# Optimization experiments

Measured on AMD Instinct MI355X. Metric: run time of the kernel, lower is better.

The kernel has to match this reference:

```python
import jax, jax.numpy as jnp
import numpy as np

B, S, I, H = 64, 1024, 512, 512


def setup_inputs() -> dict:
    key = jax.random.key(0)
    ks = jax.random.split(key, 6)
    stdv = 1.0 / np.sqrt(H)
    return {
        "inputs": jax.random.normal(ks[0], (B, S, I), dtype=jnp.float32),
        "h0": jax.random.normal(ks[1], (1, B, H), dtype=jnp.float32),
        "weight_ih": jax.random.uniform(ks[2], (H, I), jnp.float32, -stdv, stdv),
        "weight_hh": jax.random.uniform(ks[3], (H, H), jnp.float32, -stdv, stdv),
        "bias_ih": jax.random.uniform(ks[4], (H,), jnp.float32, -stdv, stdv),
        "bias_hh": jax.random.uniform(ks[5], (H,), jnp.float32, -stdv, stdv),
    }


def reference(inputs, h0, weight_ih, weight_hh, bias_ih, bias_hh):
    batch = inputs.shape[0]
    hidd = bias_hh.shape[0]
    # Precompute the input projection for all timesteps in one big GEMM:
    # [B, S, I] @ [I, H] -> [B, S, H], plus both biases.
    x_proj = jnp.einsum("bsi,hi->bsh", inputs, weight_ih) + bias_ih + bias_hh
    h_init = h0.reshape(batch, hidd)

    def step(h_prev, xp_t):  # xp_t: [B, H]
        h_t = jax.nn.relu(xp_t + h_prev @ weight_hh.T)
        return h_t, h_t

    h_final, outs = jax.lax.scan(step, h_init, jnp.swapaxes(x_proj, 0, 1))
    outputs = jnp.swapaxes(outs, 0, 1)  # [B, S, H]
    return outputs, h_final[None, :, :]
```

## Files before the change

kernel.cpp:

```cpp
#include <hip/hip_runtime.h>

#define B_ 64
#define S_ 1024
#define I_ 512
#define H_ 512
#define SH_ (S_ * H_)
#define OUT_H (B_ * SH_)

__global__ __launch_bounds__(256) void xproj_kernel(
    const float* __restrict__ A, const float* __restrict__ W,
    const float* __restrict__ bih, const float* __restrict__ bhh,
    float* __restrict__ out)
{
  __shared__ float As[16][132];
  __shared__ float Bs[16][132];
  const int tid = threadIdx.x;
  const int m0 = blockIdx.x * 128;
  const int n0 = blockIdx.y * 128;

  float acc[8][8];
  #pragma unroll
  for (int i = 0; i < 8; ++i)
    #pragma unroll
    for (int j = 0; j < 8; ++j) acc[i][j] = 0.f;

  const int mb = (tid >> 4) * 8;
  const int nb = (tid & 15) * 8;

  for (int kb = 0; kb < I_ / 16; ++kb) {
    const int k0 = kb * 16;
    __syncthreads();
    #pragma unroll
    for (int l = 0; l < 2; ++l) {
      int s  = tid + l * 256;
      int ml = s >> 2;
      int kc = s & 3;
      float4 av = *(const float4*)(A + (size_t)(m0 + ml) * I_ + k0 + kc * 4);
      As[kc*4+0][ml] = av.x; As[kc*4+1][ml] = av.y;
      As[kc*4+2][ml] = av.z; As[kc*4+3][ml] = av.w;
      float4 bv = *(const float4*)(W + (size_t)(n0 + ml) * I_ + k0 + kc * 4);
      Bs[kc*4+0][ml] = bv.x; Bs[kc*4+1][ml] = bv.y;
      Bs[kc*4+2][ml] = bv.z; Bs[kc*4+3][ml] = bv.w;
    }
    __syncthreads();
    #pragma unroll
    for (int k = 0; k < 16; ++k) {
      float4 a0 = *(const float4*)&As[k][mb];
      float4 a1 = *(const float4*)&As[k][mb + 4];
      float4 b0 = *(const float4*)&Bs[k][nb];
      float4 b1 = *(const float4*)&Bs[k][nb + 4];
      float a[8] = {a0.x,a0.y,a0.z,a0.w,a1.x,a1.y,a1.z,a1.w};
      float b[8] = {b0.x,b0.y,b0.z,b0.w,b1.x,b1.y,b1.z,b1.w};
      #pragma unroll
      for (int i = 0; i < 8; ++i)
        #pragma unroll
        for (int j = 0; j < 8; ++j) acc[i][j] += a[i] * b[j];
    }
  }

  float bias[8];
  #pragma unroll
  for (int j = 0; j < 8; ++j) bias[j] = bih[n0 + nb + j] + bhh[n0 + nb + j];
  #pragma unroll
  for (int i = 0; i < 8; ++i) {
    float4 v0 = make_float4(acc[i][0]+bias[0], acc[i][1]+bias[1],
                            acc[i][2]+bias[2], acc[i][3]+bias[3]);
    float4 v1 = make_float4(acc[i][4]+bias[4], acc[i][5]+bias[5],
                            acc[i][6]+bias[6], acc[i][7]+bias[7]);
    float* o = out + (size_t)(m0 + mb + i) * H_ + n0 + nb;
    *(float4*)o       = v0;
    *(float4*)(o + 4) = v1;
  }
}

__global__ __launch_bounds__(256) void init_kernel(unsigned* __restrict__ hbu)
{
  int i = blockIdx.x * 256 + threadIdx.x;
  if (i < B_ * H_) hbu[i] = 0u;
}

__global__ __launch_bounds__(512, 1) void recur_kernel(
    const float* __restrict__ Whh, const float* __restrict__ h0,
    float* __restrict__ out, unsigned* __restrict__ hbu)
{
  const int tid   = threadIdx.x;
  const int bg    = blockIdx.x & 31;
  const int ns    = blockIdx.x >> 5;
  const int b0    = bg * 2;
  const int obase = ns * 64;
  const int o4    = tid & 15;
  const int kq    = tid >> 4;

  __shared__ float hsh[2 * H_];
  __shared__ float red[32][132];

  float Wr[4][16];
  #pragma unroll
  for (int i = 0; i < 4; ++i) {
    const float4* wrow =
        (const float4*)(Whh + (size_t)(obase + o4 * 4 + i) * H_ + kq * 16);
    #pragma unroll
    for (int j = 0; j < 4; ++j) {
      float4 w4 = wrow[j];
      Wr[i][4*j+0] = w4.x; Wr[i][4*j+1] = w4.y;
      Wr[i][4*j+2] = w4.z; Wr[i][4*j+3] = w4.w;
    }
  }

  const int ep   = tid >> 6;
  const int lane = tid & 63;
  float* outp = out + (size_t)(b0 + ep) * SH_ + obase + lane;

  for (int t = 0; t < S_; ++t) {
    float xp = 0.f;
    if (tid < 128) xp = *outp;

    if (t == 0) {
      const float* hp = h0 + b0 * H_;
      hsh[tid]       = hp[tid];
      hsh[tid + 512] = hp[tid + 512];
    } else {
      const unsigned* hs = hbu + (t & 1) * (B_ * H_) + b0 * H_;
      const unsigned expct = ((unsigned)t >> 1) & 1u;
      unsigned a0 = __hip_atomic_load(hs + tid,       __ATOMIC_RELAXED,
                                      __HIP_MEMORY_SCOPE_AGENT);
      unsigned a1 = __hip_atomic_load(hs + tid + 512, __ATOMIC_RELAXED,
                                      __HIP_MEMORY_SCOPE_AGENT);
      while ((a0 >> 31) != expct) {
        __builtin_amdgcn_s_sleep(1);
        a0 = __hip_atomic_load(hs + tid, __ATOMIC_RELAXED,
                               __HIP_MEMORY_SCOPE_AGENT);
      }
      while ((a1 >> 31) != expct) {
        __builtin_amdgcn_s_sleep(1);
        a1 = __hip_atomic_load(hs + tid + 512, __ATOMIC_RELAXED,
                               __HIP_MEMORY_SCOPE_AGENT);
      }
      hsh[tid]       = __uint_as_float(a0 & 0x7fffffffu);
      hsh[tid + 512] = __uint_as_float(a1 & 0x7fffffffu);
    }
    __syncthreads();

    float acc[2][4] = {{0.f,0.f,0.f,0.f},{0.f,0.f,0.f,0.f}};
    #pragma unroll
    for (int b = 0; b < 2; ++b) {
      const float* hp = hsh + b * H_ + kq * 16;
      #pragma unroll
      for (int j = 0; j < 16; ++j) {
        float hv = hp[j];
        #pragma unroll
        for (int i = 0; i < 4; ++i) acc[b][i] += hv * Wr[i][j];
      }
    }

    #pragma unroll
    for (int b = 0; b < 2; ++b)
      *(float4*)&red[kq][b * 64 + o4 * 4] =
          make_float4(acc[b][0], acc[b][1], acc[b][2], acc[b][3]);
    __syncthreads();

    if (tid < 128) {
      float s = 0.f;
      #pragma unroll
      for (int q = 0; q < 32; ++q) s += red[q][ep * 64 + lane];
      float v = xp + s;
      v = v > 0.f ? v : 0.f;
      const unsigned tg = ((((unsigned)(t + 1)) >> 1) & 1u) << 31;
      unsigned* hd = hbu + ((t + 1) & 1) * (B_ * H_) + (b0 + ep) * H_
                   + obase + lane;
      __hip_atomic_store(hd, __float_as_uint(v) | tg,
                         __ATOMIC_RELAXED, __HIP_MEMORY_SCOPE_AGENT);
      *outp = v;
      if (t == S_ - 1)
        out[(size_t)OUT_H + (b0 + ep) * H_ + obase + lane] = v;
      outp += H_;
    }
  }
}

extern "C" void kernel_launch(void* const* d_in, const int* in_sizes, int n_in,
                              void* d_out, int out_size, void* d_ws, size_t ws_size,
                              hipStream_t stream)
{
  const float* inputs = (const float*)d_in[0];
  const float* h0     = (const float*)d_in[1];
  const float* w_ih   = (const float*)d_in[2];
  const float* w_hh   = (const float*)d_in[3];
  const float* b_ih   = (const float*)d_in[4];
  const float* b_hh   = (const float*)d_in[5];
  float* out = (float*)d_out;

  unsigned* hbu = (unsigned*)d_ws;

  dim3 g1(512, 4);
  xproj_kernel<<<g1, 256, 0, stream>>>(inputs, w_ih, b_ih, b_hh, out);
  init_kernel<<<128, 256, 0, stream>>>(hbu);
  recur_kernel<<<256, 512, 0, stream>>>(w_hh, h0, out, hbu);
}
```

Baseline: 2.236 ms.

## Restructure recurrence so each wavefront owns one batch row and reduces via shuffles

The recurrent kernel is remapped so each block handles a single batch row and each wavefront independently computes 16 output features over the full hidden dimension. Every wave polls and loads the whole previous hidden vector into its own shared-memory slice, and the K-split partial sums are combined with cross-lane shuffles. This removes both block-wide __syncthreads and the shared-memory reduction from every timestep. In exchange each wave issues eight times more polling loads, the register-held weight slice doubles in size, and launch bounds now target two blocks per CU.

Result: slower. 6.587 ms (+194.6%).

```diff
diff --git a/kernel.cpp b/kernel.cpp
--- a/kernel.cpp
+++ b/kernel.cpp
@@ -79,100 +79,114 @@
   if (i < B_ * H_) hbu[i] = 0u;
 }
 
-__global__ __launch_bounds__(512, 1) void recur_kernel(
+__global__ __launch_bounds__(512, 2) void recur_kernel(
     const float* __restrict__ Whh, const float* __restrict__ h0,
     float* __restrict__ out, unsigned* __restrict__ hbu)
 {
   const int tid   = threadIdx.x;
-  const int bg    = blockIdx.x & 31;
-  const int ns    = blockIdx.x >> 5;
-  const int b0    = bg * 2;
-  const int obase = ns * 64;
-  const int o4    = tid & 15;
-  const int kq    = tid >> 4;
-
-  __shared__ float hsh[2 * H_];
-  __shared__ float red[32][132];
-
-  float Wr[4][16];
+  const int lane  = tid & 63;
+  const int w     = tid >> 6;
+  const int b     = blockIdx.x & 63;
+  const int sub   = blockIdx.x >> 6;
+  const int wv    = sub * 8 + w;
+  const int obase = wv * 16;
+  const int og    = lane & 3;
+  const int kg    = lane >> 2;
+
+  __shared__ float hsh[8][16 * 36];
+
+  float Wr[4][32];
   #pragma unroll
   for (int i = 0; i < 4; ++i) {
     const float4* wrow =
-        (const float4*)(Whh + (size_t)(obase + o4 * 4 + i) * H_ + kq * 16);
-    #pragma unroll
-    for (int j = 0; j < 4; ++j) {
+        (const float4*)(Whh + (size_t)(obase + og * 4 + i) * H_ + kg * 32);
+    #pragma unroll
+    for (int j = 0; j < 8; ++j) {
       float4 w4 = wrow[j];
       Wr[i][4*j+0] = w4.x; Wr[i][4*j+1] = w4.y;
       Wr[i][4*j+2] = w4.z; Wr[i][4*j+3] = w4.w;
     }
   }
 
-  const int ep   = tid >> 6;
-  const int lane = tid & 63;
-  float* outp = out + (size_t)(b0 + ep) * SH_ + obase + lane;
+  float* hls  = &hsh[w][0];
+  float* outp = out + (size_t)b * SH_ + obase + og * 4;
 
   for (int t = 0; t < S_; ++t) {
-    float xp = 0.f;
-    if (tid < 128) xp = *outp;
+    float4 xp = make_float4(0.f, 0.f, 0.f, 0.f);
+    if (lane < 4) xp = *(const float4*)outp;
 
     if (t == 0) {
-      const float* hp = h0 + b0 * H_;
-      hsh[tid]       = hp[tid];
-      hsh[tid + 512] = hp[tid + 512];
+      const float* hp = h0 + b * H_;
+      #pragma unroll
+      for (int j = 0; j < 8; ++j) {
+        int e = lane + 64 * j;
+        hls[(e >> 5) * 36 + (e & 31)] = hp[e];
+      }
     } else {
-      const unsigned* hs = hbu + (t & 1) * (B_ * H_) + b0 * H_;
+      const unsigned* hs = hbu + (t & 1) * (B_ * H_) + b * H_;
       const unsigned expct = ((unsigned)t >> 1) & 1u;
-      unsigned a0 = __hip_atomic_load(hs + tid,       __ATOMIC_RELAXED,
-                                      __HIP_MEMORY_SCOPE_AGENT);
-      unsigned a1 = __hip_atomic_load(hs + tid + 512, __ATOMIC_RELAXED,
-                                      __HIP_MEMORY_SCOPE_AGENT);
-      while ((a0 >> 31) != expct) {
-        __builtin_amdgcn_s_sleep(1);
-        a0 = __hip_atomic_load(hs + tid, __ATOMIC_RELAXED,
-                               __HIP_MEMORY_SCOPE_AGENT);
+      unsigned a[8];
+      #pragma unroll
+      for (int j = 0; j < 8; ++j)
+        a[j] = __hip_atomic_load(hs + lane + 64 * j, __ATOMIC_RELAXED,
+                                 __HIP_MEMORY_SCOPE_AGENT);
+      #pragma unroll
+      for (int j = 0; j < 8; ++j) {
+        while ((a[j] >> 31) != expct) {
+          __builtin_amdgcn_s_sleep(1);
+          a[j] = __hip_atomic_load(hs + lane + 64 * j, __ATOMIC_RELAXED,
+                                   __HIP_MEMORY_SCOPE_AGENT);
+        }
+        int e = lane + 64 * j;
+        hls[(e >> 5) * 36 + (e & 31)] = __uint_as_float(a[j] & 0x7fffffffu);
       }
-      while ((a1 >> 31) != expct) {
-        __builtin_amdgcn_s_sleep(1);
-        a1 = __hip_atomic_load(hs + tid + 512, __ATOMIC_RELAXED,
-                               __HIP_MEMORY_SCOPE_AGENT);
+    }
+    asm volatile("s_waitcnt lgkmcnt(0)" ::: "memory");
+
+    float ac[4] = {0.f, 0.f, 0.f, 0.f};
+    const float* hc = hls + kg * 36;
+    #pragma unroll
+    for (int j4 = 0; j4 < 8; ++j4) {
+      float4 hv = *(const float4*)(hc + 4 * j4);
+      #pragma unroll
+      for (int i = 0; i < 4; ++i) {
+        ac[i] += hv.x * Wr[i][4*j4+0];
+        ac[i] += hv.y * Wr[i][4*j4+1];
+        ac[i] += hv.z * Wr[i][4*j4+2];
+        ac[i] += hv.w * Wr[i][4*j4+3];
       }
-      hsh[tid]       = __uint_as_float(a0 & 0x7fffffffu);
-      hsh[tid + 512] = __uint_as_float(a1 & 0x7fffffffu);
-    }
-    __syncthreads();
-
-    float acc[2][4] = {{0.f,0.f,0.f,0.f},{0.f,0.f,0.f,0.f}};
-    #pragma unroll
-    for (int b = 0; b < 2; ++b) {
-      const float* hp = hsh + b * H_ + kq * 16;
-      #pragma unroll
-      for (int j = 0; j < 16; ++j) {
-        float hv = hp[j];
-        #pragma unroll
-        for (int i = 0; i < 4; ++i) acc[b][i] += hv * Wr[i][j];
-      }
-    }
-
-    #pragma unroll
-    for (int b = 0; b < 2; ++b)
-      *(float4*)&red[kq][b * 64 + o4 * 4] =
-          make_float4(acc[b][0], acc[b][1], acc[b][2], acc[b][3]);
-    __syncthreads();
-
-    if (tid < 128) {
-      float s = 0.f;
-      #pragma unroll
-      for (int q = 0; q < 32; ++q) s += red[q][ep * 64 + lane];
-      float v = xp + s;
-      v = v > 0.f ? v : 0.f;
+    }
+
+    #pragma unroll
+    for (int i = 0; i < 4; ++i) {
+      float r = ac[i];
+      r += __shfl_xor(r, 4);
+      r += __shfl_xor(r, 8);
+      r += __shfl_xor(r, 16);
+      r += __shfl_xor(r, 32);
+      ac[i] = r;
+    }
+
+    if (lane < 4) {
+      float4 v;
+      v.x = fmaxf(xp.x + ac[0], 0.f);
+      v.y = fmaxf(xp.y + ac[1], 0.f);
+      v.z = fmaxf(xp.z + ac[2], 0.f);
+      v.w = fmaxf(xp.w + ac[3], 0.f);
       const unsigned tg = ((((unsigned)(t + 1)) >> 1) & 1u) << 31;
-      unsigned* hd = hbu + ((t + 1) & 1) * (B_ * H_) + (b0 + ep) * H_
-                   + obase + lane;
-      __hip_atomic_store(hd, __float_as_uint(v) | tg,
-                         __ATOMIC_RELAXED, __HIP_MEMORY_SCOPE_AGENT);
-      *outp = v;
+      unsigned* hd = hbu + ((t + 1) & 1) * (B_ * H_) + b * H_
+                   + obase + og * 4;
+      __hip_atomic_store(hd + 0, __float_as_uint(v.x) | tg,
+                         __ATOMIC_RELAXED, __HIP_MEMORY_SCOPE_AGENT);
+      __hip_atomic_store(hd + 1, __float_as_uint(v.y) | tg,
+                         __ATOMIC_RELAXED, __HIP_MEMORY_SCOPE_AGENT);
+      __hip_atomic_store(hd + 2, __float_as_uint(v.z) | tg,
+                         __ATOMIC_RELAXED, __HIP_MEMORY_SCOPE_AGENT);
+      __hip_atomic_store(hd + 3, __float_as_uint(v.w) | tg,
+                         __ATOMIC_RELAXED, __HIP_MEMORY_SCOPE_AGENT);
+      *(float4*)outp = v;
       if (t == S_ - 1)
-        out[(size_t)OUT_H + (b0 + ep) * H_ + obase + lane] = v;
+        *(float4*)(out + (size_t)OUT_H + b * H_ + obase + og * 4) = v;
       outp += H_;
     }
   }
```

## Restructure recurrent kernel to per-wave 4x4 tiles with DPP reductions

Applied to the files above, without the earlier changes.

Reworks the persistent recurrence kernel so each block handles 4 batches by 32 outputs and each wave owns 4 output rows across the full K dimension. Weights stay in registers, each lane covers 8 K values, and the partial sums are reduced inside the wave with DPP row sums plus a small per-wave LDS combine. This replaces the second block-wide __syncthreads and the 32-way shared-memory reduction. The h buffer in LDS is double-buffered and padded to avoid a barrier and bank conflicts, though relying on intra-wave LDS ordering without a barrier carries some risk.

Measured after the change: 5.276 ms. 136% more time.

```diff
diff --git a/kernel.cpp b/kernel.cpp
--- a/kernel.cpp
+++ b/kernel.cpp
@@ -6,6 +6,7 @@
 #define H_ 512
 #define SH_ (S_ * H_)
 #define OUT_H (B_ * SH_)
+#define BH_ (B_ * H_)
 
 __global__ __launch_bounds__(256) void xproj_kernel(
     const float* __restrict__ A, const float* __restrict__ W,
@@ -76,103 +77,158 @@
 __global__ __launch_bounds__(256) void init_kernel(unsigned* __restrict__ hbu)
 {
   int i = blockIdx.x * 256 + threadIdx.x;
-  if (i < B_ * H_) hbu[i] = 0u;
-}
+  if (i < BH_) hbu[i] = 0u;
+}
+
+template <int CTRL>
+__device__ __forceinline__ float dpp_add(float x) {
+  return x + __int_as_float(__builtin_amdgcn_update_dpp(
+      0, __float_as_int(x), CTRL, 0xF, 0xF, true));
+}
+__device__ __forceinline__ float rowsum16(float x) {
+  x = dpp_add<0xB1>(x);
+  x = dpp_add<0x4E>(x);
+  x = dpp_add<0x141>(x);
+  x = dpp_add<0x140>(x);
+  return x;
+}
+
+#define FMA4(A, W4, s) \
+  A.x += W4.x * (s); A.y += W4.y * (s); A.z += W4.z * (s); A.w += W4.w * (s)
+#define FMA8(A, L, Hh) \
+  FMA4(A, wv0, L.x);  FMA4(A, wv1, L.y);  FMA4(A, wv2, L.z);  FMA4(A, wv3, L.w); \
+  FMA4(A, wv4, Hh.x); FMA4(A, wv5, Hh.y); FMA4(A, wv6, Hh.z); FMA4(A, wv7, Hh.w)
 
 __global__ __launch_bounds__(512, 1) void recur_kernel(
     const float* __restrict__ Whh, const float* __restrict__ h0,
     float* __restrict__ out, unsigned* __restrict__ hbu)
 {
-  const int tid   = threadIdx.x;
-  const int bg    = blockIdx.x & 31;
-  const int ns    = blockIdx.x >> 5;
-  const int b0    = bg * 2;
-  const int obase = ns * 64;
-  const int o4    = tid & 15;
-  const int kq    = tid >> 4;
-
-  __shared__ float hsh[2 * H_];
-  __shared__ float red[32][132];
-
-  float Wr[4][16];
-  #pragma unroll
-  for (int i = 0; i < 4; ++i) {
-    const float4* wrow =
-        (const float4*)(Whh + (size_t)(obase + o4 * 4 + i) * H_ + kq * 16);
-    #pragma unroll
-    for (int j = 0; j < 4; ++j) {
-      float4 w4 = wrow[j];
-      Wr[i][4*j+0] = w4.x; Wr[i][4*j+1] = w4.y;
-      Wr[i][4*j+2] = w4.z; Wr[i][4*j+3] = w4.w;
-    }
-  }
-
-  const int ep   = tid >> 6;
+  const int tid  = threadIdx.x;
   const int lane = tid & 63;
-  float* outp = out + (size_t)(b0 + ep) * SH_ + obase + lane;
+  const int w    = tid >> 6;
+  const int bg   = blockIdx.x & 15;
+  const int ns   = blockIdx.x >> 4;
+  const int b0   = bg * 4;
+  const int ob   = ns * 32 + w * 4;
+
+  __shared__ float hsh[2][64 * 36];
+  __shared__ float redw[8][64];
+
+  const float* wp = Whh + (size_t)ob * H_ + lane * 8;
+  float4 r0a = *(const float4*)(wp           );
+  float4 r0b = *(const float4*)(wp        + 4);
+  float4 r1a = *(const float4*)(wp +   H_    );
+  float4 r1b = *(const float4*)(wp +   H_ + 4);
+  float4 r2a = *(const float4*)(wp + 2*H_    );
+  float4 r2b = *(const float4*)(wp + 2*H_ + 4);
+  float4 r3a = *(const float4*)(wp + 3*H_    );
+  float4 r3b = *(const float4*)(wp + 3*H_ + 4);
+  float4 wv0 = make_float4(r0a.x, r1a.x, r2a.x, r3a.x);
+  float4 wv1 = make_float4(r0a.y, r1a.y, r2a.y, r3a.y);
+  float4 wv2 = make_float4(r0a.z, r1a.z, r2a.z, r3a.z);
+  float4 wv3 = make_float4(r0a.w, r1a.w, r2a.w, r3a.w);
+  float4 wv4 = make_float4(r0b.x, r1b.x, r2b.x, r3b.x);
+  float4 wv5 = make_float4(r0b.y, r1b.y, r2b.y, r3b.y);
+  float4 wv6 = make_float4(r0b.z, r1b.z, r2b.z, r3b.z);
+  float4 wv7 = make_float4(r0b.w, r1b.w, r2b.w, r3b.w);
+
+  const int swb = (tid >> 3) * 36 + (tid & 7);
+
+  const int fb = b0 + ((lane >> 2) & 3);
+  const int fo = ob + (lane & 3);
+  float* outp = out + (size_t)fb * SH_ + fo;
+  unsigned* hdb = hbu + (size_t)fb * H_ + fo;
 
   for (int t = 0; t < S_; ++t) {
     float xp = 0.f;
-    if (tid < 128) xp = *outp;
-
+    if (lane < 16) xp = *outp;
+
+    float* hb = &hsh[t & 1][0];
     if (t == 0) {
-      const float* hp = h0 + b0 * H_;
-      hsh[tid]       = hp[tid];
-      hsh[tid + 512] = hp[tid + 512];
+      const float* hp = h0 + (size_t)b0 * H_ + tid;
+      hb[swb     ] = hp[0];
+      hb[swb +  8] = hp[H_];
+      hb[swb + 16] = hp[2 * H_];
+      hb[swb + 24] = hp[3 * H_];
     } else {
-      const unsigned* hs = hbu + (t & 1) * (B_ * H_) + b0 * H_;
+      const unsigned* hs = hbu + (t & 1) * BH_ + (size_t)b0 * H_ + tid;
       const unsigned expct = ((unsigned)t >> 1) & 1u;
-      unsigned a0 = __hip_atomic_load(hs + tid,       __ATOMIC_RELAXED,
-                                      __HIP_MEMORY_SCOPE_AGENT);
-      unsigned a1 = __hip_atomic_load(hs + tid + 512, __ATOMIC_RELAXED,
-                                      __HIP_MEMORY_SCOPE_AGENT);
+      unsigned a0 = __hip_atomic_load(hs,        __ATOMIC_RELAXED, __HIP_MEMORY_SCOPE_AGENT);
+      unsigned a1 = __hip_atomic_load(hs +   H_, __ATOMIC_RELAXED, __HIP_MEMORY_SCOPE_AGENT);
+      unsigned a2 = __hip_atomic_load(hs + 2*H_, __ATOMIC_RELAXED, __HIP_MEMORY_SCOPE_AGENT);
+      unsigned a3 = __hip_atomic_load(hs + 3*H_, __ATOMIC_RELAXED, __HIP_MEMORY_SCOPE_AGENT);
       while ((a0 >> 31) != expct) {
         __builtin_amdgcn_s_sleep(1);
-        a0 = __hip_atomic_load(hs + tid, __ATOMIC_RELAXED,
-                               __HIP_MEMORY_SCOPE_AGENT);
+        a0 = __hip_atomic_load(hs,        __ATOMIC_RELAXED, __HIP_MEMORY_SCOPE_AGENT);
       }
       while ((a1 >> 31) != expct) {
         __builtin_amdgcn_s_sleep(1);
-        a1 = __hip_atomic_load(hs + tid + 512, __ATOMIC_RELAXED,
-                               __HIP_MEMORY_SCOPE_AGENT);
-      }
-      hsh[tid]       = __uint_as_float(a0 & 0x7fffffffu);
-      hsh[tid + 512] = __uint_as_float(a1 & 0x7fffffffu);
+        a1 = __hip_atomic_load(hs +   H_, __ATOMIC_RELAXED, __HIP_MEMORY_SCOPE_AGENT);
+      }
+      while ((a2 >> 31) != expct) {
+        __builtin_amdgcn_s_sleep(1);
+        a2 = __hip_atomic_load(hs + 2*H_, __ATOMIC_RELAXED, __HIP_MEMORY_SCOPE_AGENT);
+      }
+      while ((a3 >> 31) != expct) {
+        __builtin_amdgcn_s_sleep(1);
+        a3 = __hip_atomic_load(hs + 3*H_, __ATOMIC_RELAXED, __HIP_MEMORY_SCOPE_AGENT);
+      }
+      hb[swb     ] = __uint_as_float(a0 & 0x7fffffffu);
+      hb[swb +  8] = __uint_as_float(a1 & 0x7fffffffu);
+      hb[swb + 16] = __uint_as_float(a2 & 0x7fffffffu);
+      hb[swb + 24] = __uint_as_float(a3 & 0x7fffffffu);
     }
     __syncthreads();
 
-    float acc[2][4] = {{0.f,0.f,0.f,0.f},{0.f,0.f,0.f,0.f}};
-    #pragma unroll
-    for (int b = 0; b < 2; ++b) {
-      const float* hp = hsh + b * H_ + kq * 16;
-      #pragma unroll
-      for (int j = 0; j < 16; ++j) {
-        float hv = hp[j];
-        #pragma unroll
-        for (int i = 0; i < 4; ++i) acc[b][i] += hv * Wr[i][j];
-      }
-    }
-
-    #pragma unroll
-    for (int b = 0; b < 2; ++b)
-      *(float4*)&red[kq][b * 64 + o4 * 4] =
-          make_float4(acc[b][0], acc[b][1], acc[b][2], acc[b][3]);
-    __syncthreads();
-
-    if (tid < 128) {
-      float s = 0.f;
-      #pragma unroll
-      for (int q = 0; q < 32; ++q) s += red[q][ep * 64 + lane];
-      float v = xp + s;
-      v = v > 0.f ? v : 0.f;
+    const float* hr = hb + lane * 36;
+    float4 hA0 = *(const float4*)(hr     );
+    float4 hA1 = *(const float4*)(hr +  4);
+    float4 hB0 = *(const float4*)(hr +  8);
+    float4 hB1 = *(const float4*)(hr + 12);
+    float4 hC0 = *(const float4*)(hr + 16);
+    float4 hC1 = *(const float4*)(hr + 20);
+    float4 hD0 = *(const float4*)(hr + 24);
+    float4 hD1 = *(const float4*)(hr + 28);
+
+    float4 aA = make_float4(0.f, 0.f, 0.f, 0.f);
+    float4 aB = make_float4(0.f, 0.f, 0.f, 0.f);
+    float4 aC = make_float4(0.f, 0.f, 0.f, 0.f);
+    float4 aD = make_float4(0.f, 0.f, 0.f, 0.f);
+    FMA8(aA, hA0, hA1);
+    FMA8(aB, hB0, hB1);
+    FMA8(aC, hC0, hC1);
+    FMA8(aD, hD0, hD1);
+
+    aA.x = rowsum16(aA.x); aA.y = rowsum16(aA.y);
+    aA.z = rowsum16(aA.z); aA.w = rowsum16(aA.w);
+    aB.x = rowsum16(aB.x); aB.y = rowsum16(aB.y);
+    aB.z = rowsum16(aB.z); aB.w = rowsum16(aB.w);
+    aC.x = rowsum16(aC.x); aC.y = rowsum16(aC.y);
+    aC.z = rowsum16(aC.z); aC.w = rowsum16(aC.w);
+    aD.x = rowsum16(aD.x); aD.y = rowsum16(aD.y);
+    aD.z = rowsum16(aD.z); aD.w = rowsum16(aD.w);
+
+    const int sa = lane & 15;
+    float4 ab = (sa >> 2) == 0 ? aA : (sa >> 2) == 1 ? aB
+              : (sa >> 2) == 2 ? aC : aD;
+    float sel = (sa & 3) == 0 ? ab.x : (sa & 3) == 1 ? ab.y
+              : (sa & 3) == 2 ? ab.z : ab.w;
+    redw[w][lane] = sel;
+    asm volatile("s_waitcnt lgkmcnt(0)" ::: "memory");
+    __builtin_amdgcn_sched_barrier(0);
+
+    if (lane < 16) {
+      float s = redw[w][lane] + redw[w][lane + 16]
+              + redw[w][lane + 32] + redw[w][lane + 48];
+      float pre = xp + s;
+      float v = pre > 0.f ? pre : 0.f;
       const unsigned tg = ((((unsigned)(t + 1)) >> 1) & 1u) << 31;
-      unsigned* hd = hbu + ((t + 1) & 1) * (B_ * H_) + (b0 + ep) * H_
-                   + obase + lane;
-      __hip_atomic_store(hd, __float_as_uint(v) | tg,
+      __hip_atomic_store(hdb + ((t + 1) & 1) * BH_,
+                         (__float_as_uint(v) & 0x7fffffffu) | tg,
                          __ATOMIC_RELAXED, __HIP_MEMORY_SCOPE_AGENT);
       *outp = v;
       if (t == S_ - 1)
-        out[(size_t)OUT_H + (b0 + ep) * H_ + obase + lane] = v;
+        out[(size_t)OUT_H + (size_t)fb * H_ + fo] = v;
       outp += H_;
     }
   }
```
